# Performance work log

Measured on AMD Instinct MI355X. Metric: run time of the kernel, lower is better.

## Reference

```python
import jax, jax.numpy as jnp
import numpy as np

NUM_USERS = 100000
NUM_ITEMS = 10000
USER_DIM = 32
ITEM_DIM = 32
H1 = 128
H2 = 128
BATCH = 4096


def setup_inputs() -> dict:
    key = jax.random.key(0)
    ks = jax.random.split(key, 10)
    interactions = jax.random.randint(ks[0], (BATCH, 2), 0, NUM_ITEMS, dtype=jnp.int64)
    users_emb_w = jax.random.normal(ks[1], (NUM_USERS, USER_DIM), dtype=jnp.float32)
    items_emb_w = jax.random.normal(ks[2], (NUM_ITEMS, ITEM_DIM), dtype=jnp.float32)
    d_in = USER_DIM + ITEM_DIM
    w1 = jax.random.normal(ks[3], (H1, d_in), dtype=jnp.float32) / np.sqrt(d_in)
    b1 = jnp.zeros((H1,), dtype=jnp.float32)
    w2 = jax.random.normal(ks[4], (H2, H1), dtype=jnp.float32) / np.sqrt(H1)
    b2 = jnp.zeros((H2,), dtype=jnp.float32)
    head_in = NUM_ITEMS + H2
    w_head = jax.random.normal(ks[5], (NUM_ITEMS, head_in), dtype=jnp.float32) / np.sqrt(head_in)
    b_head = jnp.zeros((NUM_ITEMS,), dtype=jnp.float32)
    return {
        "interactions": interactions,
        "users_emb_w": users_emb_w,
        "items_emb_w": items_emb_w,
        "w1": w1, "b1": b1, "w2": w2, "b2": b2,
        "w_head": w_head, "b_head": b_head,
    }


def reference(interactions, users_emb_w, items_emb_w, w1, b1, w2, b2, w_head, b_head):
    users = interactions[:, 0]
    items = interactions[:, 1]
    # embedding lookups + concat -> [B, 64]
    all_embed = jnp.concatenate([users_emb_w[users], items_emb_w[items]], axis=1)
    # deep MLP (dropout p=0 -> identity)
    h = jax.nn.relu(all_embed @ w1.T + b1)
    h = jax.nn.relu(h @ w2.T + b2)
    # wide one-hot [B, num_items]
    cross = jax.nn.one_hot(items, NUM_ITEMS, dtype=h.dtype)
    head_in = jnp.concatenate([cross, h], axis=1)
    return jax.nn.sigmoid(head_in @ w_head.T + b_head)
```

## Files before the change

### kernel.cpp

```cpp
#include <hip/hip_runtime.h>


#define BATCH    4096
#define NITEMS   10000
#define HEADCOLS 10128
#define DENSEOFF 10000

typedef __attribute__((ext_vector_type(8))) short short8;
typedef __attribute__((ext_vector_type(4))) short short4v;
typedef __attribute__((ext_vector_type(4))) float floatx4;

__device__ inline unsigned short f2bf(float f) {
    unsigned u = __builtin_bit_cast(unsigned, f);
    unsigned r = (u + 0x7FFFu + ((u >> 16) & 1u)) >> 16;
    return (unsigned short)r;
}

__device__ inline float bf2f(unsigned short u) {
    unsigned x = ((unsigned)u) << 16;
    return __builtin_bit_cast(float, x);
}

__global__ __launch_bounds__(256) void k1_mlp(
    const int* __restrict__ inter,
    const float* __restrict__ U, const float* __restrict__ I,
    const float* __restrict__ w1, const float* __restrict__ b1,
    const float* __restrict__ w2, const float* __restrict__ b2,
    unsigned short* __restrict__ h2b)
{
    __shared__ float e_lds[16 * 64];
    __shared__ float h1_lds[16 * 128];
    const int t  = threadIdx.x;
    const int b0 = blockIdx.x * 16;

    for (int idx = t; idx < 16 * 64; idx += 256) {
        int b = idx >> 6, d = idx & 63;
        int u  = inter[2 * (b0 + b)];
        int it = inter[2 * (b0 + b) + 1];
        e_lds[idx] = (d < 32) ? U[(long)u * 32 + d] : I[(long)it * 32 + (d - 32)];
    }
    __syncthreads();

    {
        const int i  = t & 127;
        const int bh = (t >> 7) * 8;
        float acc[8];
        #pragma unroll
        for (int b = 0; b < 8; b++) acc[b] = b1[i];
        for (int d = 0; d < 64; d += 4) {
            float4 w = *(const float4*)&w1[i * 64 + d];
            #pragma unroll
            for (int b = 0; b < 8; b++) {
                const float* e = &e_lds[(bh + b) * 64 + d];
                acc[b] += w.x * e[0] + w.y * e[1] + w.z * e[2] + w.w * e[3];
            }
        }
        #pragma unroll
        for (int b = 0; b < 8; b++) h1_lds[(bh + b) * 128 + i] = fmaxf(acc[b], 0.f);
    }
    __syncthreads();

    {
        const int o  = t & 127;
        const int bh = (t >> 7) * 8;
        float acc[8];
        #pragma unroll
        for (int b = 0; b < 8; b++) acc[b] = b2[o];
        for (int k = 0; k < 128; k += 4) {
            float4 w = *(const float4*)&w2[o * 128 + k];
            #pragma unroll
            for (int b = 0; b < 8; b++) {
                const float* h = &h1_lds[(bh + b) * 128 + k];
                acc[b] += w.x * h[0] + w.y * h[1] + w.z * h[2] + w.w * h[3];
            }
        }
        #pragma unroll
        for (int b = 0; b < 8; b++)
            h2b[(long)(b0 + bh + b) * 128 + o] = f2bf(fmaxf(acc[b], 0.f));
    }
}

#define KG_ROWS 8
__global__ __launch_bounds__(256) void kg_gather(
    const int* __restrict__ inter,
    const float* __restrict__ w_head,
    unsigned short* __restrict__ wg)
{
    const int t  = threadIdx.x;
    const int j0 = blockIdx.x * KG_ROWS;

    int c[16];
    #pragma unroll
    for (int i = 0; i < 16; i++) c[i] = inter[2 * (t + 256 * i) + 1];

    for (int r = 0; r < KG_ROWS; r++) {
        const float* row = w_head + (long)(j0 + r) * HEADCOLS;
        unsigned short* wr = wg + (long)(j0 + r) * BATCH;
        float w[16];
        #pragma unroll
        for (int i = 0; i < 16; i++) w[i] = row[c[i]];
        #pragma unroll
        for (int i = 0; i < 16; i++)
            __builtin_nontemporal_store(f2bf(w[i]), &wr[t + 256 * i]);
    }
}

#define LDSTR 136

__global__ __launch_bounds__(256) void k2_head(
    const unsigned short* __restrict__ h2b,
    const float* __restrict__ w_head, const float* __restrict__ b_head,
    const unsigned short* __restrict__ wg, float* __restrict__ out)
{
    __shared__ short A_lds[128 * LDSTR];
    __shared__ short B_lds[128 * LDSTR];

    const int t     = threadIdx.x;
    const int bbase = blockIdx.x * 128;
    const int jbase = blockIdx.y * 128;

    for (int idx = t; idx < 128 * 16; idx += 256) {
        int r = idx >> 4, s = idx & 15;
        short8 v = *(const short8*)&h2b[(long)(bbase + r) * 128 + s * 8];
        *(short8*)&A_lds[r * LDSTR + s * 8] = v;
    }
    for (int idx = t; idx < 128 * 32; idx += 256) {
        int r = idx >> 5, s = idx & 31;
        int j = jbase + r;
        short4v o4;
        if (j < NITEMS) {
            float4 w = *(const float4*)&w_head[(long)j * HEADCOLS + DENSEOFF + s * 4];
            o4[0] = (short)f2bf(w.x); o4[1] = (short)f2bf(w.y);
            o4[2] = (short)f2bf(w.z); o4[3] = (short)f2bf(w.w);
        } else {
            o4[0] = 0; o4[1] = 0; o4[2] = 0; o4[3] = 0;
        }
        *(short4v*)&B_lds[r * LDSTR + s * 4] = o4;
    }
    __syncthreads();

    const int lane = t & 63, wave = t >> 6;
    const int wb = (wave & 1) * 64, wj = (wave >> 1) * 64;
    const int col = lane & 15, quad = lane >> 4;

    floatx4 acc[4][4];
    #pragma unroll
    for (int bi = 0; bi < 4; bi++)
        #pragma unroll
        for (int ji = 0; ji < 4; ji++)
            #pragma unroll
            for (int r = 0; r < 4; r++) acc[bi][ji][r] = 0.f;

    #pragma unroll
    for (int ks = 0; ks < 4; ks++) {
        short8 a[4], b[4];
        #pragma unroll
        for (int bi = 0; bi < 4; bi++)
            a[bi] = *(const short8*)&A_lds[(wb + bi * 16 + col) * LDSTR + ks * 32 + quad * 8];
        #pragma unroll
        for (int ji = 0; ji < 4; ji++)
            b[ji] = *(const short8*)&B_lds[(wj + ji * 16 + col) * LDSTR + ks * 32 + quad * 8];
        #pragma unroll
        for (int bi = 0; bi < 4; bi++)
            #pragma unroll
            for (int ji = 0; ji < 4; ji++)
                acc[bi][ji] = __builtin_amdgcn_mfma_f32_16x16x32_bf16(a[bi], b[ji], acc[bi][ji], 0, 0, 0);
    }

    #pragma unroll
    for (int ji = 0; ji < 4; ji++) {
        int j = jbase + wj + ji * 16 + col;
        bool jv = (j < NITEMS);
        float bias = jv ? b_head[j] : 0.f;
        const unsigned short* wgr = wg + (long)(jv ? j : 0) * BATCH + bbase;
        #pragma unroll
        for (int bi = 0; bi < 4; bi++) {
            short4v wv = *(const short4v*)&wgr[wb + bi * 16 + quad * 4];
            #pragma unroll
            for (int r = 0; r < 4; r++) {
                int bl = wb + bi * 16 + quad * 4 + r;
                float wide = bf2f((unsigned short)wv[r]);
                float x = acc[bi][ji][r] + bias + wide;
                float y = 1.f / (1.f + __expf(-x));
                if (jv) __builtin_nontemporal_store(y, &out[(long)(bbase + bl) * NITEMS + j]);
            }
        }
    }
}

__global__ __launch_bounds__(256) void k2_head_fb(
    const unsigned short* __restrict__ h2b,
    const float* __restrict__ w_head, const float* __restrict__ b_head,
    const int* __restrict__ inter, float* __restrict__ out)
{
    __shared__ short A_lds[128 * LDSTR];
    __shared__ short B_lds[128 * LDSTR];
    __shared__ int items[128];

    const int t     = threadIdx.x;
    const int bbase = blockIdx.x * 128;
    const int jbase = blockIdx.y * 128;

    if (t < 128) items[t] = inter[2 * (bbase + t) + 1];

    for (int idx = t; idx < 128 * 16; idx += 256) {
        int r = idx >> 4, s = idx & 15;
        short8 v = *(const short8*)&h2b[(long)(bbase + r) * 128 + s * 8];
        *(short8*)&A_lds[r * LDSTR + s * 8] = v;
    }
    for (int idx = t; idx < 128 * 32; idx += 256) {
        int r = idx >> 5, s = idx & 31;
        int j = jbase + r;
        short4v o4;
        if (j < NITEMS) {
            float4 w = *(const float4*)&w_head[(long)j * HEADCOLS + DENSEOFF + s * 4];
            o4[0] = (short)f2bf(w.x); o4[1] = (short)f2bf(w.y);
            o4[2] = (short)f2bf(w.z); o4[3] = (short)f2bf(w.w);
        } else {
            o4[0] = 0; o4[1] = 0; o4[2] = 0; o4[3] = 0;
        }
        *(short4v*)&B_lds[r * LDSTR + s * 4] = o4;
    }
    __syncthreads();

    const int lane = t & 63, wave = t >> 6;
    const int wb = (wave & 1) * 64, wj = (wave >> 1) * 64;
    const int col = lane & 15, quad = lane >> 4;

    floatx4 acc[4][4];
    #pragma unroll
    for (int bi = 0; bi < 4; bi++)
        #pragma unroll
        for (int ji = 0; ji < 4; ji++)
            #pragma unroll
            for (int r = 0; r < 4; r++) acc[bi][ji][r] = 0.f;

    #pragma unroll
    for (int ks = 0; ks < 4; ks++) {
        short8 a[4], b[4];
        #pragma unroll
        for (int bi = 0; bi < 4; bi++)
            a[bi] = *(const short8*)&A_lds[(wb + bi * 16 + col) * LDSTR + ks * 32 + quad * 8];
        #pragma unroll
        for (int ji = 0; ji < 4; ji++)
            b[ji] = *(const short8*)&B_lds[(wj + ji * 16 + col) * LDSTR + ks * 32 + quad * 8];
        #pragma unroll
        for (int bi = 0; bi < 4; bi++)
            #pragma unroll
            for (int ji = 0; ji < 4; ji++)
                acc[bi][ji] = __builtin_amdgcn_mfma_f32_16x16x32_bf16(a[bi], b[ji], acc[bi][ji], 0, 0, 0);
    }

    #pragma unroll
    for (int ji = 0; ji < 4; ji++) {
        int j = jbase + wj + ji * 16 + col;
        bool jv = (j < NITEMS);
        float bias = jv ? b_head[j] : 0.f;
        const float* wrow = w_head + (long)(jv ? j : 0) * HEADCOLS;
        #pragma unroll
        for (int bi = 0; bi < 4; bi++) {
            #pragma unroll
            for (int r = 0; r < 4; r++) {
                int bl = wb + bi * 16 + quad * 4 + r;
                float wide = jv ? wrow[items[bl]] : 0.f;
                float x = acc[bi][ji][r] + bias + wide;
                float y = 1.f / (1.f + __expf(-x));
                if (jv) out[(long)(bbase + bl) * NITEMS + j] = y;
            }
        }
    }
}

extern "C" void kernel_launch(void* const* d_in, const int* in_sizes, int n_in,
                              void* d_out, int out_size, void* d_ws, size_t ws_size,
                              hipStream_t stream) {
    const int*   inter = (const int*)d_in[0];
    const float* U     = (const float*)d_in[1];
    const float* I     = (const float*)d_in[2];
    const float* w1    = (const float*)d_in[3];
    const float* b1    = (const float*)d_in[4];
    const float* w2    = (const float*)d_in[5];
    const float* b2    = (const float*)d_in[6];
    const float* wh    = (const float*)d_in[7];
    const float* bh    = (const float*)d_in[8];
    float* out = (float*)d_out;

    unsigned short* h2b = (unsigned short*)d_ws;
    const size_t WG_OFF  = 1u << 20;
    const size_t WG_SIZE = (size_t)NITEMS * BATCH * 2;

    k1_mlp<<<256, 256, 0, stream>>>(inter, U, I, w1, b1, w2, b2, h2b);

    if (ws_size >= WG_OFF + WG_SIZE) {
        unsigned short* wg = (unsigned short*)((char*)d_ws + WG_OFF);
        kg_gather<<<NITEMS / KG_ROWS, 256, 0, stream>>>(inter, wh, wg);
        k2_head<<<dim3(32, 79), 256, 0, stream>>>(h2b, wh, bh, wg, out);
    } else {
        k2_head_fb<<<dim3(32, 79), 256, 0, stream>>>(h2b, wh, bh, inter, out);
    }
}
```

Baseline: 793.7 us.

## Stream head rows through LDS for gather and pre-convert dense head weights

The gather kernel now loads each w_head row coalesced into LDS with non-temporal loads and does the per-item gather from LDS. It packs two bf16 outputs per 32-bit store and also writes a bf16 copy of the 128 dense columns per row. k2_head then reads these prepacked bf16 dense weights instead of converting fp32 rows itself. The MLP kernel is re-split to 8 batch rows per block across 512 blocks and uses float4 LDS reads. The aim is to replace scattered global gathers with full-row streaming, at the cost of reading the whole 400MB w_head and some extra workspace.

```diff
diff --git a/kernel.cpp b/kernel.cpp
--- a/kernel.cpp
+++ b/kernel.cpp
@@ -28,12 +28,12 @@
     const float* __restrict__ w2, const float* __restrict__ b2,
     unsigned short* __restrict__ h2b)
 {
-    __shared__ float e_lds[16 * 64];
-    __shared__ float h1_lds[16 * 128];
+    __shared__ float e_lds[8 * 64];
+    __shared__ float h1_lds[8 * 128];
     const int t  = threadIdx.x;
-    const int b0 = blockIdx.x * 16;
-
-    for (int idx = t; idx < 16 * 64; idx += 256) {
+    const int b0 = blockIdx.x * 8;
+
+    for (int idx = t; idx < 8 * 64; idx += 256) {
         int b = idx >> 6, d = idx & 63;
         int u  = inter[2 * (b0 + b)];
         int it = inter[2 * (b0 + b) + 1];
@@ -41,67 +41,80 @@
     }
     __syncthreads();
 
+    const int i = t & 127;
+    const int g = (t >> 7) * 4;
+
     {
-        const int i  = t & 127;
-        const int bh = (t >> 7) * 8;
-        float acc[8];
-        #pragma unroll
-        for (int b = 0; b < 8; b++) acc[b] = b1[i];
+        float acc[4];
+        #pragma unroll
+        for (int b = 0; b < 4; b++) acc[b] = b1[i];
         for (int d = 0; d < 64; d += 4) {
             float4 w = *(const float4*)&w1[i * 64 + d];
             #pragma unroll
-            for (int b = 0; b < 8; b++) {
-                const float* e = &e_lds[(bh + b) * 64 + d];
-                acc[b] += w.x * e[0] + w.y * e[1] + w.z * e[2] + w.w * e[3];
+            for (int b = 0; b < 4; b++) {
+                float4 e = *(const float4*)&e_lds[(g + b) * 64 + d];
+                acc[b] += w.x * e.x + w.y * e.y + w.z * e.z + w.w * e.w;
             }
         }
         #pragma unroll
-        for (int b = 0; b < 8; b++) h1_lds[(bh + b) * 128 + i] = fmaxf(acc[b], 0.f);
+        for (int b = 0; b < 4; b++) h1_lds[(g + b) * 128 + i] = fmaxf(acc[b], 0.f);
     }
     __syncthreads();
 
     {
-        const int o  = t & 127;
-        const int bh = (t >> 7) * 8;
-        float acc[8];
-        #pragma unroll
-        for (int b = 0; b < 8; b++) acc[b] = b2[o];
+        float acc[4];
+        #pragma unroll
+        for (int b = 0; b < 4; b++) acc[b] = b2[i];
         for (int k = 0; k < 128; k += 4) {
-            float4 w = *(const float4*)&w2[o * 128 + k];
-            #pragma unroll
-            for (int b = 0; b < 8; b++) {
-                const float* h = &h1_lds[(bh + b) * 128 + k];
-                acc[b] += w.x * h[0] + w.y * h[1] + w.z * h[2] + w.w * h[3];
+            float4 w = *(const float4*)&w2[i * 128 + k];
+            #pragma unroll
+            for (int b = 0; b < 4; b++) {
+                float4 h = *(const float4*)&h1_lds[(g + b) * 128 + k];
+                acc[b] += w.x * h.x + w.y * h.y + w.z * h.z + w.w * h.w;
             }
         }
         #pragma unroll
-        for (int b = 0; b < 8; b++)
-            h2b[(long)(b0 + bh + b) * 128 + o] = f2bf(fmaxf(acc[b], 0.f));
-    }
-}
-
-#define KG_ROWS 8
+        for (int b = 0; b < 4; b++)
+            h2b[(long)(b0 + g + b) * 128 + i] = f2bf(fmaxf(acc[b], 0.f));
+    }
+}
+
+#define KG_ROWS 4
 __global__ __launch_bounds__(256) void kg_gather(
     const int* __restrict__ inter,
     const float* __restrict__ w_head,
-    unsigned short* __restrict__ wg)
+    unsigned short* __restrict__ wg,
+    unsigned short* __restrict__ wd)
 {
+    __shared__ float row_lds[HEADCOLS];
     const int t  = threadIdx.x;
     const int j0 = blockIdx.x * KG_ROWS;
 
-    int c[16];
-    #pragma unroll
-    for (int i = 0; i < 16; i++) c[i] = inter[2 * (t + 256 * i) + 1];
+    int c0[8], c1[8];
+    #pragma unroll
+    for (int i = 0; i < 8; i++) {
+        int p = t + 256 * i;
+        c0[i] = inter[4 * p + 1];
+        c1[i] = inter[4 * p + 3];
+    }
 
     for (int r = 0; r < KG_ROWS; r++) {
         const float* row = w_head + (long)(j0 + r) * HEADCOLS;
-        unsigned short* wr = wg + (long)(j0 + r) * BATCH;
-        float w[16];
-        #pragma unroll
-        for (int i = 0; i < 16; i++) w[i] = row[c[i]];
-        #pragma unroll
-        for (int i = 0; i < 16; i++)
-            __builtin_nontemporal_store(f2bf(w[i]), &wr[t + 256 * i]);
+        for (int idx = t; idx < HEADCOLS / 4; idx += 256) {
+            floatx4 v = __builtin_nontemporal_load((const floatx4*)row + idx);
+            *(floatx4*)&row_lds[idx * 4] = v;
+        }
+        __syncthreads();
+
+        unsigned* wr = (unsigned*)(wg + (long)(j0 + r) * BATCH);
+        #pragma unroll
+        for (int i = 0; i < 8; i++) {
+            unsigned lo = f2bf(row_lds[c0[i]]);
+            unsigned hi = f2bf(row_lds[c1[i]]);
+            __builtin_nontemporal_store(lo | (hi << 16), &wr[t + 256 * i]);
+        }
+        if (t < 128) wd[(long)(j0 + r) * 128 + t] = f2bf(row_lds[DENSEOFF + t]);
+        __syncthreads();
     }
 }
 
@@ -109,7 +122,7 @@
 
 __global__ __launch_bounds__(256) void k2_head(
     const unsigned short* __restrict__ h2b,
-    const float* __restrict__ w_head, const float* __restrict__ b_head,
+    const unsigned short* __restrict__ wd, const float* __restrict__ b_head,
     const unsigned short* __restrict__ wg, float* __restrict__ out)
 {
     __shared__ short A_lds[128 * LDSTR];
@@ -124,18 +137,13 @@
         short8 v = *(const short8*)&h2b[(long)(bbase + r) * 128 + s * 8];
         *(short8*)&A_lds[r * LDSTR + s * 8] = v;
     }
-    for (int idx = t; idx < 128 * 32; idx += 256) {
-        int r = idx >> 5, s = idx & 31;
+    for (int idx = t; idx < 128 * 16; idx += 256) {
+        int r = idx >> 4, s = idx & 15;
         int j = jbase + r;
-        short4v o4;
-        if (j < NITEMS) {
-            float4 w = *(const float4*)&w_head[(long)j * HEADCOLS + DENSEOFF + s * 4];
-            o4[0] = (short)f2bf(w.x); o4[1] = (short)f2bf(w.y);
-            o4[2] = (short)f2bf(w.z); o4[3] = (short)f2bf(w.w);
-        } else {
-            o4[0] = 0; o4[1] = 0; o4[2] = 0; o4[3] = 0;
-        }
-        *(short4v*)&B_lds[r * LDSTR + s * 4] = o4;
+        short8 v;
+        if (j < NITEMS) v = *(const short8*)&wd[(long)j * 128 + s * 8];
+        else { v[0]=0;v[1]=0;v[2]=0;v[3]=0;v[4]=0;v[5]=0;v[6]=0;v[7]=0; }
+        *(short8*)&B_lds[r * LDSTR + s * 8] = v;
     }
     __syncthreads();
 
@@ -288,13 +296,16 @@
     unsigned short* h2b = (unsigned short*)d_ws;
     const size_t WG_OFF  = 1u << 20;
     const size_t WG_SIZE = (size_t)NITEMS * BATCH * 2;
-
-    k1_mlp<<<256, 256, 0, stream>>>(inter, U, I, w1, b1, w2, b2, h2b);
-
-    if (ws_size >= WG_OFF + WG_SIZE) {
+    const size_t WD_OFF  = WG_OFF + WG_SIZE;
+    const size_t WD_SIZE = (size_t)NITEMS * 128 * 2;
+
+    k1_mlp<<<512, 256, 0, stream>>>(inter, U, I, w1, b1, w2, b2, h2b);
+
+    if (ws_size >= WD_OFF + WD_SIZE) {
         unsigned short* wg = (unsigned short*)((char*)d_ws + WG_OFF);
-        kg_gather<<<NITEMS / KG_ROWS, 256, 0, stream>>>(inter, wh, wg);
-        k2_head<<<dim3(32, 79), 256, 0, stream>>>(h2b, wh, bh, wg, out);
+        unsigned short* wd = (unsigned short*)((char*)d_ws + WD_OFF);
+        kg_gather<<<NITEMS / KG_ROWS, 256, 0, stream>>>(inter, wh, wg, wd);
+        k2_head<<<dim3(32, 79), 256, 0, stream>>>(h2b, wd, bh, wg, out);
     } else {
         k2_head_fb<<<dim3(32, 79), 256, 0, stream>>>(h2b, wh, bh, inter, out);
     }
```

Result: faster. 691.3 us (-12.9%).
